# Performance work log

Hardware: AMD Instinct MI355X
Metric: run time of the kernel (lower is better)

Reference implementation:

```python
import jax, jax.numpy as jnp
import numpy as np

N_NODES = 100000
N_EDGES = 1600000
IN_FEATS = 64
HIDDEN = 64
NUM_CLASSES = 2


def setup_inputs() -> dict:
    key = jax.random.key(0)
    ks = jax.random.split(key, 9)
    feat = jax.random.normal(ks[0], (N_NODES, IN_FEATS), dtype=jnp.float32)
    src = jax.random.randint(ks[1], (N_EDGES,), 0, N_NODES, dtype=jnp.int64) if jax.config.jax_enable_x64 else jax.random.randint(ks[1], (N_EDGES,), 0, N_NODES).astype(jnp.int32)
    dst = jax.random.randint(ks[2], (N_EDGES,), 0, N_NODES).astype(src.dtype)
    s_in = 1.0 / np.sqrt(IN_FEATS)
    s_e = 1.0 / np.sqrt(2 * HIDDEN)
    s_o = 1.0 / np.sqrt(HIDDEN)
    W_in = jax.random.uniform(ks[3], (IN_FEATS, HIDDEN), jnp.float32, -s_in, s_in)
    b_in = jax.random.uniform(ks[4], (HIDDEN,), jnp.float32, -s_in, s_in)
    W_edge = jax.random.uniform(ks[5], (2 * HIDDEN, 1), jnp.float32, -s_e, s_e)
    b_edge = jax.random.uniform(ks[6], (1,), jnp.float32, -s_e, s_e)
    W_out = jax.random.uniform(ks[7], (HIDDEN, NUM_CLASSES), jnp.float32, -s_o, s_o)
    b_out = jax.random.uniform(ks[8], (NUM_CLASSES,), jnp.float32, -s_o, s_o)
    return {"feat": feat, "src": src, "dst": dst, "W_in": W_in, "b_in": b_in,
            "W_edge": W_edge, "b_edge": b_edge, "W_out": W_out, "b_out": b_out}


def reference(feat, src, dst, W_in, b_in, W_edge, b_edge, W_out, b_out):
    # input node MLP: [N, in] @ [in, H]
    h = feat @ W_in + b_in  # [N, H]
    # edge function: sigmoid(Linear(cat(h_src, h_dst))) -- split concat to avoid [E, 2H] buffer
    hu = h[src]  # [E, H]
    hv = h[dst]  # [E, H]
    W_u, W_v = W_edge[:HIDDEN], W_edge[HIDDEN:]  # each [H, 1]
    w = jax.nn.sigmoid(hu @ W_u + hv @ W_v + b_edge)  # [E, 1]
    # message = h_src * w, reduce = sum over incoming edges at dst
    msgs = hu * w  # [E, H]
    agg = jax.ops.segment_sum(msgs, dst, num_segments=N_NODES)  # [N, H]
    # DGL UDF-reduce semantics: zero in-degree nodes keep previous h
    deg = jax.ops.segment_sum(jnp.ones((dst.shape[0],), dtype=jnp.float32), dst, num_segments=N_NODES)
    h_new = jnp.where(deg[:, None] > 0, agg, h)
    return h_new @ W_out + b_out  # [N, num_classes]
```

## Files before the change

kernel.cpp:

```cpp
#include <hip/hip_runtime.h>
#include <math.h>

#define N_NODES 100000
#define N_EDGES 1600000

#define BK_LOG 7
#define BKW 128
#define NBK ((N_NODES + BKW - 1) / BKW)
#define CAPB 2688
#define UNS4 3

#define GS 128
#define EPS (N_EDGES / GS)
#define EPS4 (EPS / 4)
#define SROUNDS ((EPS4 + 255) / 256)

#define NT_BLOCKS ((N_NODES + 63) / 64)

__global__ __launch_bounds__(256) void prep_kernel(
    const float* __restrict__ feat,
    const float* __restrict__ W_in,
    const float* __restrict__ b_in,
    const float* __restrict__ W_edge,
    const float* __restrict__ W_out,
    const int*   __restrict__ src,
    const int*   __restrict__ dst,
    int* __restrict__ cursor,
    int* __restrict__ ework,
    float4* __restrict__ nodeT)
{
    const int tid = threadIdx.x;

    if ((int)blockIdx.x < GS) {
        __shared__ int hist[NBK];
        __shared__ int rhist[NBK];
        __shared__ int gbase[NBK];
        for (int i = tid; i < NBK; i += 256) { hist[i] = 0; rhist[i] = 0; }
        __syncthreads();

        const int4* src4 = (const int4*)src;
        const int4* dst4 = (const int4*)dst;
        const int   b40  = (int)blockIdx.x * EPS4;

        for (int j = 0; j < SROUNDS; ++j) {
            const int o4 = j * 256 + tid;
            if (o4 < EPS4) {
                const int4 d4 = dst4[b40 + o4];
                atomicAdd(&hist[d4.x >> BK_LOG], 1);
                atomicAdd(&hist[d4.y >> BK_LOG], 1);
                atomicAdd(&hist[d4.z >> BK_LOG], 1);
                atomicAdd(&hist[d4.w >> BK_LOG], 1);
            }
        }
        __syncthreads();

        for (int i = tid; i < NBK; i += 256) {
            const int c = hist[i];
            if (c) gbase[i] = atomicAdd(&cursor[i], c);
        }
        __syncthreads();

        for (int j = 0; j < SROUNDS; ++j) {
            const int o4 = j * 256 + tid;
            if (o4 < EPS4) {
                const int4 d4 = dst4[b40 + o4];
                const int4 s4 = src4[b40 + o4];
                const int dv[4] = {d4.x, d4.y, d4.z, d4.w};
                const int sv[4] = {s4.x, s4.y, s4.z, s4.w};
                #pragma unroll
                for (int u = 0; u < 4; ++u) {
                    const int d = dv[u];
                    const int b = d >> BK_LOG;
                    const int r = atomicAdd(&rhist[b], 1);
                    ework[b * CAPB + gbase[b] + r] =
                        ((d & (BKW - 1)) << 17) | sv[u];
                }
            }
        }
        return;
    }

    __shared__ float sP[64 * 4];
    __shared__ float sQ[64 * 4];
    __shared__ float sc[4];

    if (tid < 64) {
        sP[tid * 4 + 0] = W_edge[tid];
        sP[tid * 4 + 1] = W_out[tid * 2 + 0];
        sP[tid * 4 + 2] = W_out[tid * 2 + 1];
        sP[tid * 4 + 3] = W_edge[64 + tid];
    }
    __syncthreads();

    {
        const int k = tid >> 2, j = tid & 3;
        float q = 0.f;
        for (int m = 0; m < 64; ++m) q += W_in[k * 64 + m] * sP[m * 4 + j];
        sQ[k * 4 + j] = q;
        if (tid < 4) {
            float cc = 0.f;
            for (int m = 0; m < 64; ++m) cc += b_in[m] * sP[m * 4 + tid];
            sc[tid] = cc;
        }
    }
    __syncthreads();

    const int lane = tid & 63;
    const int wv   = tid >> 6;
    const int n    = ((int)blockIdx.x - GS) * 64 + wv * 16 + (lane >> 2);
    const int ks   = (lane & 3) << 4;

    float p0 = 0.f, p1 = 0.f, p2 = 0.f, p3 = 0.f;
    if (n < N_NODES) {
        const float* fr = feat + (size_t)n * 64 + ks;
        #pragma unroll
        for (int i4 = 0; i4 < 4; ++i4) {
            const float4 f = *(const float4*)(fr + i4 * 4);
            const float fv[4] = {f.x, f.y, f.z, f.w};
            #pragma unroll
            for (int u = 0; u < 4; ++u) {
                const float4 q = *(const float4*)&sQ[(ks + i4 * 4 + u) * 4];
                p0 += fv[u] * q.x;
                p1 += fv[u] * q.y;
                p2 += fv[u] * q.z;
                p3 += fv[u] * q.w;
            }
        }
    }
    #pragma unroll
    for (int off = 1; off <= 2; off <<= 1) {
        p0 += __shfl_xor(p0, off);
        p1 += __shfl_xor(p1, off);
        p2 += __shfl_xor(p2, off);
        p3 += __shfl_xor(p3, off);
    }
    if (n < N_NODES && (lane & 3) == 0)
        nodeT[n] = make_float4(p0 + sc[0], p1 + sc[1], p2 + sc[2], p3 + sc[3]);
}

__global__ __launch_bounds__(256) void agg_kernel(
    const int* __restrict__ ework,
    const int* __restrict__ cursor,
    const float4* __restrict__ nodeT,
    const float* __restrict__ b_edge,
    const float* __restrict__ b_out,
    float2* __restrict__ out)
{
    __shared__ float4 sT[BKW];
    __shared__ float  aM0[BKW];
    __shared__ float  aM1[BKW];
    __shared__ int    aC[BKW];

    const int b   = blockIdx.x;
    const int tid = threadIdx.x;

    if (tid < BKW) {
        const int n = b * BKW + tid;
        float4 t = make_float4(0.f, 0.f, 0.f, 0.f);
        if (n < N_NODES) t = nodeT[n];
        t.w += b_edge[0];
        sT[tid] = t;
        aM0[tid] = 0.f;
        aM1[tid] = 0.f;
        aC[tid]  = 0;
    }
    __syncthreads();

    const int cnt = min(cursor[b], CAPB);
    const int4* ew4 = (const int4*)(ework + b * CAPB);

    #pragma unroll
    for (int j = 0; j < UNS4; ++j) {
        const int o = (j * 256 + tid) * 4;
        if (o < cnt) {
            const int4 v = ew4[j * 256 + tid];
            const int ve[4] = {v.x, v.y, v.z, v.w};
            #pragma unroll
            for (int u = 0; u < 4; ++u) {
                if (o + u < cnt) {
                    const int    l = ve[u] >> 17;
                    const int    s = ve[u] & 0x1FFFF;
                    const float4 t = nodeT[s];
                    const float  w = 1.0f / (1.0f + __expf(-(t.x + sT[l].w)));
                    atomicAdd(&aM0[l], w * t.y);
                    atomicAdd(&aM1[l], w * t.z);
                    atomicAdd(&aC[l], 1);
                }
            }
        }
    }
    __syncthreads();

    if (tid < BKW) {
        const int n = b * BKW + tid;
        if (n < N_NODES) {
            const bool has = aC[tid] > 0;
            out[n] = make_float2((has ? aM0[tid] : sT[tid].y) + b_out[0],
                                 (has ? aM1[tid] : sT[tid].z) + b_out[1]);
        }
    }
}

extern "C" void kernel_launch(void* const* d_in, const int* in_sizes, int n_in,
                              void* d_out, int out_size, void* d_ws, size_t ws_size,
                              hipStream_t stream) {
    const float* feat   = (const float*)d_in[0];
    const int*   src    = (const int*)d_in[1];
    const int*   dst    = (const int*)d_in[2];
    const float* W_in   = (const float*)d_in[3];
    const float* b_in   = (const float*)d_in[4];
    const float* W_edge = (const float*)d_in[5];
    const float* b_edge = (const float*)d_in[6];
    const float* W_out  = (const float*)d_in[7];
    const float* b_out  = (const float*)d_in[8];
    float2* out = (float2*)d_out;

    float4* nodeT  = (float4*)d_ws;
    int*    ework  = (int*)(nodeT + N_NODES);
    int*    cursor = ework + NBK * CAPB;

    hipMemsetAsync(cursor, 0, NBK * sizeof(int), stream);

    prep_kernel<<<GS + NT_BLOCKS, 256, 0, stream>>>(
        feat, W_in, b_in, W_edge, W_out, src, dst, cursor, ework, nodeT);
    agg_kernel<<<NBK, 256, 0, stream>>>(
        ework, cursor, nodeT, b_edge, b_out, out);
}
```

Before: 137.6 us.

## Replace global-cursor edge bucketing with fixed per-group slots and counts

The edge binning no longer builds a per-block histogram, takes global atomic cursors, or needs a memset. Each of 400 source groups now writes its edges for each destination bucket into a private fixed-size slot of 27 records, with the count stored in the slot header. The aggregation kernel has each thread read one group's slot with nontemporal vector loads and runs 512-thread blocks. This removes a pass over dst, the global atomics and the memset. In exchange the workspace is much larger and sparse: the aggregation kernel reads every slot in full, and edges beyond 27 per slot would be silently dropped, which is very unlikely for random inputs.

```diff
diff --git a/kernel.cpp b/kernel.cpp
--- a/kernel.cpp
+++ b/kernel.cpp
@@ -7,15 +7,17 @@
 #define BK_LOG 7
 #define BKW 128
 #define NBK ((N_NODES + BKW - 1) / BKW)
-#define CAPB 2688
-#define UNS4 3
-
-#define GS 128
+#define GS 400
 #define EPS (N_EDGES / GS)
 #define EPS4 (EPS / 4)
-#define SROUNDS ((EPS4 + 255) / 256)
+#define SR ((EPS4 + 255) / 256)
+
+#define CH 28
+#define CAPC (CH - 1)
 
 #define NT_BLOCKS ((N_NODES + 63) / 64)
+
+typedef int i32x4 __attribute__((ext_vector_type(4)));
 
 __global__ __launch_bounds__(256) void prep_kernel(
     const float* __restrict__ feat,
@@ -25,7 +27,6 @@
     const float* __restrict__ W_out,
     const int*   __restrict__ src,
     const int*   __restrict__ dst,
-    int* __restrict__ cursor,
     int* __restrict__ ework,
     float4* __restrict__ nodeT)
 {
@@ -33,34 +34,16 @@
 
     if ((int)blockIdx.x < GS) {
         __shared__ int hist[NBK];
-        __shared__ int rhist[NBK];
-        __shared__ int gbase[NBK];
-        for (int i = tid; i < NBK; i += 256) { hist[i] = 0; rhist[i] = 0; }
+        for (int i = tid; i < NBK; i += 256) hist[i] = 0;
         __syncthreads();
 
         const int4* src4 = (const int4*)src;
         const int4* dst4 = (const int4*)dst;
         const int   b40  = (int)blockIdx.x * EPS4;
-
-        for (int j = 0; j < SROUNDS; ++j) {
-            const int o4 = j * 256 + tid;
-            if (o4 < EPS4) {
-                const int4 d4 = dst4[b40 + o4];
-                atomicAdd(&hist[d4.x >> BK_LOG], 1);
-                atomicAdd(&hist[d4.y >> BK_LOG], 1);
-                atomicAdd(&hist[d4.z >> BK_LOG], 1);
-                atomicAdd(&hist[d4.w >> BK_LOG], 1);
-            }
-        }
-        __syncthreads();
-
-        for (int i = tid; i < NBK; i += 256) {
-            const int c = hist[i];
-            if (c) gbase[i] = atomicAdd(&cursor[i], c);
-        }
-        __syncthreads();
-
-        for (int j = 0; j < SROUNDS; ++j) {
+        const int   g    = (int)blockIdx.x;
+
+        #pragma unroll
+        for (int j = 0; j < SR; ++j) {
             const int o4 = j * 256 + tid;
             if (o4 < EPS4) {
                 const int4 d4 = dst4[b40 + o4];
@@ -71,12 +54,17 @@
                 for (int u = 0; u < 4; ++u) {
                     const int d = dv[u];
                     const int b = d >> BK_LOG;
-                    const int r = atomicAdd(&rhist[b], 1);
-                    ework[b * CAPB + gbase[b] + r] =
-                        ((d & (BKW - 1)) << 17) | sv[u];
+                    const int r = atomicAdd(&hist[b], 1);
+                    if (r < CAPC)
+                        ework[(b * GS + g) * CH + 1 + r] =
+                            ((d & (BKW - 1)) << 17) | sv[u];
                 }
             }
         }
+        __syncthreads();
+
+        for (int i = tid; i < NBK; i += 256)
+            ework[(i * GS + g) * CH] = min(hist[i], CAPC);
         return;
     }
 
@@ -138,9 +126,8 @@
         nodeT[n] = make_float4(p0 + sc[0], p1 + sc[1], p2 + sc[2], p3 + sc[3]);
 }
 
-__global__ __launch_bounds__(256) void agg_kernel(
+__global__ __launch_bounds__(512) void agg_kernel(
     const int* __restrict__ ework,
-    const int* __restrict__ cursor,
     const float4* __restrict__ nodeT,
     const float* __restrict__ b_edge,
     const float* __restrict__ b_out,
@@ -166,24 +153,27 @@
     }
     __syncthreads();
 
-    const int cnt = min(cursor[b], CAPB);
-    const int4* ew4 = (const int4*)(ework + b * CAPB);
-
-    #pragma unroll
-    for (int j = 0; j < UNS4; ++j) {
-        const int o = (j * 256 + tid) * 4;
-        if (o < cnt) {
-            const int4 v = ew4[j * 256 + tid];
-            const int ve[4] = {v.x, v.y, v.z, v.w};
+    if (tid < GS) {
+        const i32x4* cp = (const i32x4*)(ework + ((size_t)b * GS + tid) * CH);
+        i32x4 v[7];
+        #pragma unroll
+        for (int j = 0; j < 7; ++j) v[j] = __builtin_nontemporal_load(cp + j);
+        const int cnt = min(v[0].x, CAPC);
+
+        #pragma unroll
+        for (int j = 0; j < 7; ++j) {
+            const int ve[4] = {v[j].x, v[j].y, v[j].z, v[j].w};
             #pragma unroll
             for (int u = 0; u < 4; ++u) {
-                if (o + u < cnt) {
-                    const int    l = ve[u] >> 17;
-                    const int    s = ve[u] & 0x1FFFF;
-                    const float4 t = nodeT[s];
-                    const float  w = 1.0f / (1.0f + __expf(-(t.x + sT[l].w)));
-                    atomicAdd(&aM0[l], w * t.y);
-                    atomicAdd(&aM1[l], w * t.z);
+                const int w = j * 4 + u;
+                if (w >= 1 && w <= cnt) {
+                    const int    rec = ve[u];
+                    const int    l   = rec >> 17;
+                    const int    s   = rec & 0x1FFFF;
+                    const float4 t   = nodeT[s];
+                    const float  wg  = 1.0f / (1.0f + __expf(-(t.x + sT[l].w)));
+                    atomicAdd(&aM0[l], wg * t.y);
+                    atomicAdd(&aM1[l], wg * t.z);
                     atomicAdd(&aC[l], 1);
                 }
             }
@@ -215,14 +205,11 @@
     const float* b_out  = (const float*)d_in[8];
     float2* out = (float2*)d_out;
 
-    float4* nodeT  = (float4*)d_ws;
-    int*    ework  = (int*)(nodeT + N_NODES);
-    int*    cursor = ework + NBK * CAPB;
-
-    hipMemsetAsync(cursor, 0, NBK * sizeof(int), stream);
+    float4* nodeT = (float4*)d_ws;
+    int*    ework = (int*)(nodeT + N_NODES);
 
     prep_kernel<<<GS + NT_BLOCKS, 256, 0, stream>>>(
-        feat, W_in, b_in, W_edge, W_out, src, dst, cursor, ework, nodeT);
-    agg_kernel<<<NBK, 256, 0, stream>>>(
-        ework, cursor, nodeT, b_edge, b_out, out);
+        feat, W_in, b_in, W_edge, W_out, src, dst, ework, nodeT);
+    agg_kernel<<<NBK, 512, 0, stream>>>(
+        ework, nodeT, b_edge, b_out, out);
 }
```

Measured after the change: 146.9 us. 1.07x slower.

## Fuse histogram and rank passes, keep edge slots in registers, raise scatter blocks

Applied to the files above, without the earlier changes.

The bucket-scatter phase now reads each edge's dst/src once, taking its per-block rank from the shared histogram atomic and holding bucket, rank and packed value in registers until the global base offsets are reserved. This removes the second read of dst/src and the separate rank-counter atomics. The number of scatter blocks rises from 128 to 400, giving each thread at most 16 edges in registers, which adds parallelism at the cost of more global cursor atomics and higher register pressure.

```diff
diff --git a/kernel.cpp b/kernel.cpp
--- a/kernel.cpp
+++ b/kernel.cpp
@@ -10,10 +10,9 @@
 #define CAPB 2688
 #define UNS4 3
 
-#define GS 128
+#define GS 400
 #define EPS (N_EDGES / GS)
 #define EPS4 (EPS / 4)
-#define SROUNDS ((EPS4 + 255) / 256)
 
 #define NT_BLOCKS ((N_NODES + 63) / 64)
 
@@ -33,34 +32,17 @@
 
     if ((int)blockIdx.x < GS) {
         __shared__ int hist[NBK];
-        __shared__ int rhist[NBK];
-        __shared__ int gbase[NBK];
-        for (int i = tid; i < NBK; i += 256) { hist[i] = 0; rhist[i] = 0; }
+        __shared__ int base[NBK];
+        for (int i = tid; i < NBK; i += 256) hist[i] = 0;
         __syncthreads();
 
         const int4* src4 = (const int4*)src;
         const int4* dst4 = (const int4*)dst;
         const int   b40  = (int)blockIdx.x * EPS4;
 
-        for (int j = 0; j < SROUNDS; ++j) {
-            const int o4 = j * 256 + tid;
-            if (o4 < EPS4) {
-                const int4 d4 = dst4[b40 + o4];
-                atomicAdd(&hist[d4.x >> BK_LOG], 1);
-                atomicAdd(&hist[d4.y >> BK_LOG], 1);
-                atomicAdd(&hist[d4.z >> BK_LOG], 1);
-                atomicAdd(&hist[d4.w >> BK_LOG], 1);
-            }
-        }
-        __syncthreads();
-
-        for (int i = tid; i < NBK; i += 256) {
-            const int c = hist[i];
-            if (c) gbase[i] = atomicAdd(&cursor[i], c);
-        }
-        __syncthreads();
-
-        for (int j = 0; j < SROUNDS; ++j) {
+        int bb[16], rr[16], pk[16];
+        #pragma unroll
+        for (int j = 0; j < 4; ++j) {
             const int o4 = j * 256 + tid;
             if (o4 < EPS4) {
                 const int4 d4 = dst4[b40 + o4];
@@ -69,11 +51,31 @@
                 const int sv[4] = {s4.x, s4.y, s4.z, s4.w};
                 #pragma unroll
                 for (int u = 0; u < 4; ++u) {
+                    const int idx = j * 4 + u;
                     const int d = dv[u];
                     const int b = d >> BK_LOG;
-                    const int r = atomicAdd(&rhist[b], 1);
-                    ework[b * CAPB + gbase[b] + r] =
-                        ((d & (BKW - 1)) << 17) | sv[u];
+                    bb[idx] = b;
+                    rr[idx] = atomicAdd(&hist[b], 1);
+                    pk[idx] = ((d & (BKW - 1)) << 17) | sv[u];
+                }
+            }
+        }
+        __syncthreads();
+
+        for (int b = tid; b < NBK; b += 256) {
+            const int c = hist[b];
+            if (c) base[b] = atomicAdd(&cursor[b], c);
+        }
+        __syncthreads();
+
+        #pragma unroll
+        for (int j = 0; j < 4; ++j) {
+            const int o4 = j * 256 + tid;
+            if (o4 < EPS4) {
+                #pragma unroll
+                for (int u = 0; u < 4; ++u) {
+                    const int idx = j * 4 + u;
+                    ework[bb[idx] * CAPB + base[bb[idx]] + rr[idx]] = pk[idx];
                 }
             }
         }
```

New measurement: 142.2 us. 3.4% more time.
